# Kernel tuning notes

Measured on AMD Instinct MI355X. Metric: run time of the kernel, lower is better.

## Reference

```python
import jax, jax.numpy as jnp
import numpy as np

N_CELL, N_DRUG = 8192, 4096


def setup_inputs() -> dict:
    key = jax.random.key(0)
    adj = jax.random.uniform(key, (N_CELL, N_DRUG), dtype=jnp.float32)
    return {"adj": adj}


def reference(adj):
    # Degree normalizations with +1 self-loop smoothing, as in the torch module.
    d_x = (jnp.sum(adj, axis=1) + 1.0) ** -0.5  # [N_CELL]
    d_y = (jnp.sum(adj, axis=0) + 1.0) ** -0.5  # [N_DRUG]

    # diag(d_x) @ adj @ diag(d_y) == row/col broadcast scaling (same math, O(n^2)).
    agg_cell_lp = d_x[:, None] * adj * d_y[None, :]          # [N_CELL, N_DRUG]
    agg_drug_lp = d_y[:, None] * adj.T * d_x[None, :]        # [N_DRUG, N_CELL]

    d_c = (jnp.sum(adj, axis=1) + 1.0) ** -1.0               # [N_CELL]
    self_cell_lp = jnp.diag(d_c + 1.0)                       # [N_CELL, N_CELL]
    d_d = (jnp.sum(adj, axis=0) + 1.0) ** -1.0               # [N_DRUG]
    self_drug_lp = jnp.diag(d_d + 1.0)                       # [N_DRUG, N_DRUG]

    return (agg_cell_lp, agg_drug_lp, self_cell_lp, self_drug_lp)
```

## Files before the change

### kernel.cpp

```cpp
#include <hip/hip_runtime.h>

#define N_CELL 8192
#define N_DRUG 4096

typedef float f32x4 __attribute__((ext_vector_type(4)));

static constexpr size_t OFF1 = (size_t)N_CELL * N_DRUG;
static constexpr size_t OFF2 = 2ull * N_CELL * N_DRUG;
static constexpr size_t OFF3 = OFF2 + (size_t)N_CELL * N_CELL;

__global__ __launch_bounds__(256) void sums_kernel(const float* __restrict__ adj,
                                                   float* __restrict__ rowsum,
                                                   float* __restrict__ colsum) {
    __shared__ float part[64][65];
    int tid = threadIdx.x;
    int cb = blockIdx.x & 3;
    int rb = blockIdx.x >> 2;
    int c0 = cb * 1024;
    int r0 = rb * 64;
    const f32x4* ap = reinterpret_cast<const f32x4*>(adj + (size_t)r0 * N_DRUG + c0) + tid;
    f32x4 cacc = {0.f, 0.f, 0.f, 0.f};
#pragma unroll 4
    for (int r = 0; r < 64; ++r) {
        f32x4 v = ap[(size_t)r * (N_DRUG / 4)];
        cacc += v;
        float h = (v.x + v.y) + (v.z + v.w);
        h += __shfl_down(h, 1, 64);
        h += __shfl_down(h, 2, 64);
        if ((tid & 3) == 0) part[r][tid >> 2] = h;
    }
    __syncthreads();
    if (tid < 64) {
        float s = 0.f;
#pragma unroll 8
        for (int j = 0; j < 64; ++j) s += part[tid][j];
        atomicAdd(&rowsum[r0 + tid], s);
    }
    int c = c0 + tid * 4;
    atomicAdd(&colsum[c + 0], cacc.x);
    atomicAdd(&colsum[c + 1], cacc.y);
    atomicAdd(&colsum[c + 2], cacc.z);
    atomicAdd(&colsum[c + 3], cacc.w);
}

__global__ __launch_bounds__(256) void scale_kernel(const float* __restrict__ adj,
                                                    const float* __restrict__ rowsum,
                                                    const float* __restrict__ colsum,
                                                    float* __restrict__ out) {
    __shared__ float tile[64][69];
    int tid = threadIdx.x;
    int tx = tid & 15;
    int ty = tid >> 4;
    int c0 = blockIdx.x * 64;
    int r0 = blockIdx.y * 64;

    f32x4 cs = *reinterpret_cast<const f32x4*>(colsum + c0 + tx * 4);
    f32x4 dy;
    dy.x = rsqrtf(cs.x + 1.0f);
    dy.y = rsqrtf(cs.y + 1.0f);
    dy.z = rsqrtf(cs.z + 1.0f);
    dy.w = rsqrtf(cs.w + 1.0f);

#pragma unroll
    for (int q = 0; q < 4; ++q) {
        int rr = q * 16 + ty;
        int r = r0 + rr;
        float dx = rsqrtf(rowsum[r] + 1.0f);
        f32x4 v = *reinterpret_cast<const f32x4*>(adj + (size_t)r * N_DRUG + c0 + tx * 4);
        f32x4 o = v * dx;
        o *= dy;
        __builtin_nontemporal_store(
            o, reinterpret_cast<f32x4*>(out + (size_t)r * N_DRUG + c0 + tx * 4));
        tile[rr][tx * 4 + 0] = o.x;
        tile[rr][tx * 4 + 1] = o.y;
        tile[rr][tx * 4 + 2] = o.z;
        tile[rr][tx * 4 + 3] = o.w;
    }
    __syncthreads();
    float* aggd = out + OFF1;
#pragma unroll
    for (int q = 0; q < 4; ++q) {
        int dr = q * 16 + ty;
        f32x4 o;
        o.x = tile[tx * 4 + 0][dr];
        o.y = tile[tx * 4 + 1][dr];
        o.z = tile[tx * 4 + 2][dr];
        o.w = tile[tx * 4 + 3][dr];
        __builtin_nontemporal_store(
            o, reinterpret_cast<f32x4*>(aggd + (size_t)(c0 + dr) * N_CELL + r0 + tx * 4));
    }
}

__global__ __launch_bounds__(256) void diag_kernel(const float* __restrict__ rowsum,
                                                   const float* __restrict__ colsum,
                                                   float* __restrict__ out) {
    int i = blockIdx.x * 256 + threadIdx.x;
    if (i < N_CELL) {
        out[OFF2 + (size_t)i * (N_CELL + 1)] = 1.0f / (rowsum[i] + 1.0f) + 1.0f;
    } else if (i < N_CELL + N_DRUG) {
        int j = i - N_CELL;
        out[OFF3 + (size_t)j * (N_DRUG + 1)] = 1.0f / (colsum[j] + 1.0f) + 1.0f;
    }
}

extern "C" void kernel_launch(void* const* d_in, const int* in_sizes, int n_in,
                              void* d_out, int out_size, void* d_ws, size_t ws_size,
                              hipStream_t stream) {
    const float* adj = (const float*)d_in[0];
    float* out = (float*)d_out;
    float* rowsum = (float*)d_ws;
    float* colsum = rowsum + N_CELL;

    (void)hipMemsetAsync(d_ws, 0, (N_CELL + N_DRUG) * sizeof(float), stream);

    sums_kernel<<<512, 256, 0, stream>>>(adj, rowsum, colsum);
    scale_kernel<<<dim3(N_DRUG / 64, N_CELL / 64), 256, 0, stream>>>(adj, rowsum, colsum, out);

    (void)hipMemsetAsync(out + OFF2,
                         0,
                         ((size_t)N_CELL * N_CELL + (size_t)N_DRUG * N_DRUG) * sizeof(float),
                         stream);
    diag_kernel<<<48, 256, 0, stream>>>(rowsum, colsum, out);
}
```

Measured before the change: 176.4 us.

## Replace memset with nontemporal fill kernel, fold diag writes into larger scale blocks

```diff
diff --git a/kernel.cpp b/kernel.cpp
--- a/kernel.cpp
+++ b/kernel.cpp
@@ -8,6 +8,19 @@
 static constexpr size_t OFF1 = (size_t)N_CELL * N_DRUG;
 static constexpr size_t OFF2 = 2ull * N_CELL * N_DRUG;
 static constexpr size_t OFF3 = OFF2 + (size_t)N_CELL * N_CELL;
+static constexpr size_t FILL_F4 = ((size_t)N_CELL * N_CELL + (size_t)N_DRUG * N_DRUG) / 4;
+
+#define FILL_BLOCKS 2048
+static constexpr size_t FILL_PER_BLOCK = FILL_F4 / FILL_BLOCKS;
+
+__global__ __launch_bounds__(256) void fill_kernel(float* __restrict__ fill_base) {
+    f32x4 z = {0.f, 0.f, 0.f, 0.f};
+    f32x4* p = reinterpret_cast<f32x4*>(fill_base) + (size_t)blockIdx.x * FILL_PER_BLOCK;
+#pragma unroll 4
+    for (size_t i = threadIdx.x; i < FILL_PER_BLOCK; i += 256) {
+        __builtin_nontemporal_store(z, p + i);
+    }
+}
 
 __global__ __launch_bounds__(256) void sums_kernel(const float* __restrict__ adj,
                                                    float* __restrict__ rowsum,
@@ -43,63 +56,68 @@
     atomicAdd(&colsum[c + 3], cacc.w);
 }
 
+#define DIAG_BLOCKS 48
 __global__ __launch_bounds__(256) void scale_kernel(const float* __restrict__ adj,
                                                     const float* __restrict__ rowsum,
                                                     const float* __restrict__ colsum,
                                                     float* __restrict__ out) {
-    __shared__ float tile[64][69];
     int tid = threadIdx.x;
+    int b = blockIdx.x;
+    if (b < DIAG_BLOCKS) {
+        int idx = b * 256 + tid;
+        if (idx < N_CELL) {
+            out[OFF2 + (size_t)idx * (N_CELL + 1)] = 1.0f / (rowsum[idx] + 1.0f) + 1.0f;
+        } else {
+            int k = idx - N_CELL;
+            out[OFF3 + (size_t)k * (N_DRUG + 1)] = 1.0f / (colsum[k] + 1.0f) + 1.0f;
+        }
+        return;
+    }
+    __shared__ float lds[64][69];
+    int t = b - DIAG_BLOCKS;
     int tx = tid & 15;
     int ty = tid >> 4;
-    int c0 = blockIdx.x * 64;
-    int r0 = blockIdx.y * 64;
-
-    f32x4 cs = *reinterpret_cast<const f32x4*>(colsum + c0 + tx * 4);
-    f32x4 dy;
-    dy.x = rsqrtf(cs.x + 1.0f);
-    dy.y = rsqrtf(cs.y + 1.0f);
-    dy.z = rsqrtf(cs.z + 1.0f);
-    dy.w = rsqrtf(cs.w + 1.0f);
-
-#pragma unroll
-    for (int q = 0; q < 4; ++q) {
-        int rr = q * 16 + ty;
-        int r = r0 + rr;
-        float dx = rsqrtf(rowsum[r] + 1.0f);
-        f32x4 v = *reinterpret_cast<const f32x4*>(adj + (size_t)r * N_DRUG + c0 + tx * 4);
-        f32x4 o = v * dx;
-        o *= dy;
-        __builtin_nontemporal_store(
-            o, reinterpret_cast<f32x4*>(out + (size_t)r * N_DRUG + c0 + tx * 4));
-        tile[rr][tx * 4 + 0] = o.x;
-        tile[rr][tx * 4 + 1] = o.y;
-        tile[rr][tx * 4 + 2] = o.z;
-        tile[rr][tx * 4 + 3] = o.w;
-    }
-    __syncthreads();
+    int c0 = (t & 31) * 128;
+    int r0 = (t >> 5) * 128;
     float* aggd = out + OFF1;
 #pragma unroll
-    for (int q = 0; q < 4; ++q) {
-        int dr = q * 16 + ty;
-        f32x4 o;
-        o.x = tile[tx * 4 + 0][dr];
-        o.y = tile[tx * 4 + 1][dr];
-        o.z = tile[tx * 4 + 2][dr];
-        o.w = tile[tx * 4 + 3][dr];
-        __builtin_nontemporal_store(
-            o, reinterpret_cast<f32x4*>(aggd + (size_t)(c0 + dr) * N_CELL + r0 + tx * 4));
-    }
-}
-
-__global__ __launch_bounds__(256) void diag_kernel(const float* __restrict__ rowsum,
-                                                   const float* __restrict__ colsum,
-                                                   float* __restrict__ out) {
-    int i = blockIdx.x * 256 + threadIdx.x;
-    if (i < N_CELL) {
-        out[OFF2 + (size_t)i * (N_CELL + 1)] = 1.0f / (rowsum[i] + 1.0f) + 1.0f;
-    } else if (i < N_CELL + N_DRUG) {
-        int j = i - N_CELL;
-        out[OFF3 + (size_t)j * (N_DRUG + 1)] = 1.0f / (colsum[j] + 1.0f) + 1.0f;
+    for (int s = 0; s < 4; ++s) {
+        int cc = c0 + (s & 1) * 64;
+        int rr0 = r0 + (s >> 1) * 64;
+        f32x4 cs = *reinterpret_cast<const f32x4*>(colsum + cc + tx * 4);
+        f32x4 dy;
+        dy.x = rsqrtf(cs.x + 1.0f);
+        dy.y = rsqrtf(cs.y + 1.0f);
+        dy.z = rsqrtf(cs.z + 1.0f);
+        dy.w = rsqrtf(cs.w + 1.0f);
+#pragma unroll
+        for (int q = 0; q < 4; ++q) {
+            int rr = q * 16 + ty;
+            int r = rr0 + rr;
+            float dx = rsqrtf(rowsum[r] + 1.0f);
+            f32x4 v = *reinterpret_cast<const f32x4*>(adj + (size_t)r * N_DRUG + cc + tx * 4);
+            f32x4 o = v * dx;
+            o *= dy;
+            __builtin_nontemporal_store(
+                o, reinterpret_cast<f32x4*>(out + (size_t)r * N_DRUG + cc + tx * 4));
+            lds[rr][tx * 4 + 0] = o.x;
+            lds[rr][tx * 4 + 1] = o.y;
+            lds[rr][tx * 4 + 2] = o.z;
+            lds[rr][tx * 4 + 3] = o.w;
+        }
+        __syncthreads();
+#pragma unroll
+        for (int q = 0; q < 4; ++q) {
+            int dr = q * 16 + ty;
+            f32x4 o;
+            o.x = lds[tx * 4 + 0][dr];
+            o.y = lds[tx * 4 + 1][dr];
+            o.z = lds[tx * 4 + 2][dr];
+            o.w = lds[tx * 4 + 3][dr];
+            __builtin_nontemporal_store(
+                o, reinterpret_cast<f32x4*>(aggd + (size_t)(cc + dr) * N_CELL + rr0 + tx * 4));
+        }
+        __syncthreads();
     }
 }
 
@@ -113,12 +131,7 @@
 
     (void)hipMemsetAsync(d_ws, 0, (N_CELL + N_DRUG) * sizeof(float), stream);
 
+    fill_kernel<<<FILL_BLOCKS, 256, 0, stream>>>(out + OFF2);
     sums_kernel<<<512, 256, 0, stream>>>(adj, rowsum, colsum);
-    scale_kernel<<<dim3(N_DRUG / 64, N_CELL / 64), 256, 0, stream>>>(adj, rowsum, colsum, out);
-
-    (void)hipMemsetAsync(out + OFF2,
-                         0,
-                         ((size_t)N_CELL * N_CELL + (size_t)N_DRUG * N_DRUG) * sizeof(float),
-                         stream);
-    diag_kernel<<<48, 256, 0, stream>>>(rowsum, colsum, out);
+    scale_kernel<<<DIAG_BLOCKS + 2048, 256, 0, stream>>>(adj, rowsum, colsum, out);
 }
```

After: 174.3 us. About the same (-1.2%).
